# Kernel tuning notes

Measured on AMD Instinct MI355X. Metric: run time of the kernel, lower is better.

The kernel has to match this reference:

```python
import jax, jax.numpy as jnp
import numpy as np

D_IN = 2048
D_LATENT = 16384
BATCH = 4096
K = 64


def setup_inputs() -> dict:
    key = jax.random.key(0)
    k1, k2, k3 = jax.random.split(key, 3)
    s_enc = 1.0 / np.sqrt(D_IN)
    s_dec = 1.0 / np.sqrt(D_LATENT)
    return {
        "x": jax.random.normal(k1, (BATCH, D_IN), dtype=jnp.float32),
        "W_enc": jax.random.normal(k2, (D_LATENT, D_IN), dtype=jnp.float32) * s_enc,
        "b_enc": jnp.zeros((D_LATENT,), dtype=jnp.float32),
        "W_dec": jax.random.normal(k3, (D_IN, D_LATENT), dtype=jnp.float32) * s_dec,
        "b_dec": jnp.zeros((D_IN,), dtype=jnp.float32),
        "k": K,
    }


def reference(x, W_enc, b_enc, W_dec, b_dec, k):
    # encode: dense GEMM + ReLU  -> h: [B, d_latent]
    h = jax.nn.relu(jnp.einsum("bd,ld->bl", x, W_enc) + b_enc)
    # top-k masking over latent dim (dim=1)
    _, idx = jax.lax.top_k(h, k)  # idx: [B, k]
    B = h.shape[0]
    mask = jnp.zeros(h.shape, dtype=bool).at[jnp.arange(B)[:, None], idx].set(True)
    h_topk = jnp.where(mask, h, jnp.zeros((), dtype=h.dtype))
    # decode: GEMM through sparse latents
    x_hat = jnp.einsum("bl,dl->bd", h_topk, W_dec) + b_dec
    return x_hat, h, h_topk
```

## Files before the change

### kernel.cpp

```cpp
#include <hip/hip_runtime.h>
#include <cstdint>

#define DIN   2048
#define DLAT  16384
#define NB    4096
#define KSEL  64
#define MAXC  128

typedef unsigned short u16;
typedef unsigned int   u32;
typedef __attribute__((ext_vector_type(8))) short short8;
typedef __attribute__((ext_vector_type(4))) float f32x4;

#define GLOAD_LDS16(g, l)                                              \
    __builtin_amdgcn_global_load_lds(                                  \
        (const __attribute__((address_space(1))) void*)(g),            \
        (__attribute__((address_space(3))) void*)(l), 16, 0, 0)

__device__ __forceinline__ u32 f32_to_bf16(u32 u)
{
    u += 0x7FFFu + ((u >> 16) & 1u);
    return u >> 16;
}

__global__ __launch_bounds__(256)
void cvt_f32_bf16_kernel(const float* __restrict__ in, u16* __restrict__ out, int n8)
{
    const int i = blockIdx.x * 256 + threadIdx.x;
    if (i >= n8) return;
    const float4* p = reinterpret_cast<const float4*>(in) + (size_t)i * 2;
    const float4 a = p[0], b = p[1];
    const float v[8] = {a.x, a.y, a.z, a.w, b.x, b.y, b.z, b.w};
    u32 r[8];
#pragma unroll
    for (int j = 0; j < 8; ++j) r[j] = f32_to_bf16(__float_as_uint(v[j]));
    uint4 o;
    o.x = r[0] | (r[1] << 16);
    o.y = r[2] | (r[3] << 16);
    o.z = r[4] | (r[5] << 16);
    o.w = r[6] | (r[7] << 16);
    reinterpret_cast<uint4*>(out)[i] = o;
}

__global__ __launch_bounds__(512, 2)
void sae_encode_mfma512(const u16* __restrict__ XB, const u16* __restrict__ WB,
                        const float* __restrict__ benc, float* __restrict__ H)
{
    __shared__ __align__(16) u16 lds[2 * 16384];

    const int tid = threadIdx.x;
    const int wv  = tid >> 6;
    const int ln  = tid & 63;
    const int wm  = wv >> 2;
    const int wn  = wv & 3;
    const int fr  = ln & 15;
    const int fq  = ln >> 4;

    const int b   = blockIdx.x;
    const int wg  = (b & 7) * 128 + (b >> 3);
    const int m_blk = wg & 15;
    const int n_blk = wg >> 4;
    const size_t bm = (size_t)m_blk * 256;
    const size_t bn = (size_t)n_blk * 256;

    const int   srow  = tid >> 2;
    const int   sslot = (tid & 3) ^ ((tid >> 3) & 3);
    const u16* aS = XB + (bm + srow) * DIN + sslot * 8;
    const u16* bS = WB + (bn + srow) * DIN + sslot * 8;

    auto STAGE = [&](int kt, int bi) {
        const int c = kt * 32;
        GLOAD_LDS16(aS + c,                       &lds[bi * 16384 + wv * 512]);
        GLOAD_LDS16(aS + c + (size_t)128 * DIN,   &lds[bi * 16384 + 4096 + wv * 512]);
        GLOAD_LDS16(bS + c,                       &lds[bi * 16384 + 8192 + wv * 512]);
        GLOAD_LDS16(bS + c + (size_t)128 * DIN,   &lds[bi * 16384 + 12288 + wv * 512]);
    };

    f32x4 acc[8][4];
#pragma unroll
    for (int i = 0; i < 8; ++i)
#pragma unroll
        for (int j = 0; j < 4; ++j) acc[i][j] = (f32x4)0.0f;

    const int sw = (fq ^ ((fr >> 1) & 3)) * 8;

    STAGE(0, 0);
    asm volatile("s_waitcnt vmcnt(0)" ::: "memory");
    __builtin_amdgcn_s_barrier();
    asm volatile("" ::: "memory");

    for (int t = 0; t < 64; ++t) {
        const int rbase = (t & 1) * 16384;
        short8 a[8], bb[4];
#pragma unroll
        for (int mi = 0; mi < 8; ++mi)
            a[mi] = *reinterpret_cast<const short8*>(
                &lds[rbase + (wm * 128 + mi * 16 + fr) * 32 + sw]);
#pragma unroll
        for (int ni = 0; ni < 4; ++ni)
            bb[ni] = *reinterpret_cast<const short8*>(
                &lds[rbase + 8192 + (wn * 64 + ni * 16 + fr) * 32 + sw]);

        if (t < 63) STAGE(t + 1, (t + 1) & 1);

        __builtin_amdgcn_s_setprio(1);
#pragma unroll
        for (int mi = 0; mi < 8; ++mi)
#pragma unroll
            for (int ni = 0; ni < 4; ++ni)
                acc[mi][ni] = __builtin_amdgcn_mfma_f32_16x16x32_bf16(
                    a[mi], bb[ni], acc[mi][ni], 0, 0, 0);
        __builtin_amdgcn_s_setprio(0);

        asm volatile("s_waitcnt vmcnt(0)" ::: "memory");
        __builtin_amdgcn_s_barrier();
        asm volatile("" ::: "memory");
    }

#pragma unroll
    for (int ni = 0; ni < 4; ++ni) {
        const size_t col = bn + wn * 64 + ni * 16 + fr;
        const float be = benc[col];
#pragma unroll
        for (int mi = 0; mi < 8; ++mi) {
            const size_t r0 = bm + wm * 128 + mi * 16 + fq * 4;
            const f32x4 v = acc[mi][ni];
#pragma unroll
            for (int j = 0; j < 4; ++j)
                H[(r0 + j) * DLAT + col] = fmaxf(v[j] + be, 0.0f);
        }
    }
}

__global__ __launch_bounds__(256, 4)
void sae_encode_kernel(const float* __restrict__ X, const float* __restrict__ W,
                       const float* __restrict__ benc, float* __restrict__ H)
{
    __shared__ float As[32][132];
    __shared__ float Bs[32][132];

    const int tid  = threadIdx.x;
    const int bm   = blockIdx.y * 128;
    const int bn   = blockIdx.x * 128;

    const int wave = tid >> 6;
    const int lane = tid & 63;
    const int tm   = ((wave >> 1) << 3) + (lane >> 3);
    const int tn   = ((wave &  1) << 3) + (lane &  7);

    float acc[8][8];
#pragma unroll
    for (int i = 0; i < 8; ++i)
#pragma unroll
        for (int j = 0; j < 8; ++j) acc[i][j] = 0.0f;

    const int lrow = tid >> 1;
    const int lcol = (tid & 1) << 4;

    const float* xptr = X + (size_t)(bm + lrow) * DIN + lcol;
    const float* wptr = W + (size_t)(bn + lrow) * DIN + lcol;

    for (int k0 = 0; k0 < DIN; k0 += 32) {
#pragma unroll
        for (int i = 0; i < 4; ++i) {
            const float4 av = *reinterpret_cast<const float4*>(xptr + k0 + 4 * i);
            const float4 bv = *reinterpret_cast<const float4*>(wptr + k0 + 4 * i);
            const int kk = lcol + 4 * i;
            As[kk + 0][lrow] = av.x; As[kk + 1][lrow] = av.y;
            As[kk + 2][lrow] = av.z; As[kk + 3][lrow] = av.w;
            Bs[kk + 0][lrow] = bv.x; Bs[kk + 1][lrow] = bv.y;
            Bs[kk + 2][lrow] = bv.z; Bs[kk + 3][lrow] = bv.w;
        }
        __syncthreads();

#pragma unroll 8
        for (int k = 0; k < 32; ++k) {
            const float4 a0 = *reinterpret_cast<const float4*>(&As[k][tm * 8]);
            const float4 a1 = *reinterpret_cast<const float4*>(&As[k][tm * 8 + 4]);
            const float4 b0 = *reinterpret_cast<const float4*>(&Bs[k][tn * 8]);
            const float4 b1 = *reinterpret_cast<const float4*>(&Bs[k][tn * 8 + 4]);
            const float a[8] = {a0.x, a0.y, a0.z, a0.w, a1.x, a1.y, a1.z, a1.w};
            const float b[8] = {b0.x, b0.y, b0.z, b0.w, b1.x, b1.y, b1.z, b1.w};
#pragma unroll
            for (int i = 0; i < 8; ++i)
#pragma unroll
                for (int j = 0; j < 8; ++j)
                    acc[i][j] = fmaf(a[i], b[j], acc[i][j]);
        }
        __syncthreads();
    }

#pragma unroll
    for (int i = 0; i < 8; ++i) {
        float* orow = H + (size_t)(bm + tm * 8 + i) * DLAT + bn + tn * 8;
#pragma unroll
        for (int j = 0; j < 8; j += 4) {
            float4 o;
            o.x = fmaxf(acc[i][j + 0] + benc[bn + tn * 8 + j + 0], 0.0f);
            o.y = fmaxf(acc[i][j + 1] + benc[bn + tn * 8 + j + 1], 0.0f);
            o.z = fmaxf(acc[i][j + 2] + benc[bn + tn * 8 + j + 2], 0.0f);
            o.w = fmaxf(acc[i][j + 3] + benc[bn + tn * 8 + j + 3], 0.0f);
            *reinterpret_cast<float4*>(orow + j) = o;
        }
    }
}

__device__ __forceinline__ int blk_scan256(int v, volatile int* wsum,
                                           int ln, int wv, int& total)
{
#pragma unroll
    for (int off = 1; off < 64; off <<= 1) {
        const int n = __shfl_up(v, off, 64);
        if (ln >= off) v += n;
    }
    if (ln == 63) wsum[wv] = v;
    __syncthreads();
    int add = 0;
#pragma unroll
    for (int c = 0; c < 3; ++c) if (c < wv) add += wsum[c];
    total = wsum[0] + wsum[1] + wsum[2] + wsum[3];
    __syncthreads();
    return v + add;
}

template <bool WRITE_LISTS>
__global__ __launch_bounds__(256)
void sae_topk_kernel(const float* __restrict__ H, const float* __restrict__ X,
                     const float* __restrict__ Wenc, const float* __restrict__ benc,
                     float* __restrict__ Ht, int* __restrict__ sidx,
                     float* __restrict__ sval, float band)
{
    __shared__ __align__(16) float xs[DIN];
    __shared__ u32  hist[4][256];
    __shared__ int  scan_[256];
    __shared__ int  wsum[4];
    __shared__ int  sh_bin, sh_above;
    __shared__ int           cand_idx[MAXC];
    __shared__ float         cand_val[MAXC];
    __shared__ unsigned char cand_sel[MAXC];
    __shared__ float psum[32][6];

    const int tid = threadIdx.x;
    const int wv  = tid >> 6;
    const int ln  = tid & 63;
    const int row = blockIdx.x;
    const u32* __restrict__ hrow =
        reinterpret_cast<const u32*>(H) + (size_t)row * DLAT;

    {
        const float4* xp = reinterpret_cast<const float4*>(X + (size_t)row * DIN);
        reinterpret_cast<float4*>(xs)[tid * 2 + 0] = xp[tid * 2 + 0];
        reinterpret_cast<float4*>(xs)[tid * 2 + 1] = xp[tid * 2 + 1];
    }

    u32 v[64];
#pragma unroll
    for (int j = 0; j < 16; ++j) {
        const uint4 q = *reinterpret_cast<const uint4*>(hrow + j * 1024 + tid * 4);
        v[j * 4 + 0] = q.x; v[j * 4 + 1] = q.y;
        v[j * 4 + 2] = q.z; v[j * 4 + 3] = q.w;
    }

    u32 prefix = 0, msk = 0;
    int kk = KSEL;
    for (int pass = 0; pass < 4; ++pass) {
        const int shift = 24 - 8 * pass;
        hist[0][tid] = 0; hist[1][tid] = 0; hist[2][tid] = 0; hist[3][tid] = 0;
        __syncthreads();
#pragma unroll
        for (int e = 0; e < 64; ++e) {
            const u32 x = v[e];
            if (x != 0u && (x & msk) == prefix)
                atomicAdd(&hist[wv][(x >> shift) & 255u], 1u);
        }
        __syncthreads();
        int val = (int)(hist[0][255 - tid] + hist[1][255 - tid] +
                        hist[2][255 - tid] + hist[3][255 - tid]);
#pragma unroll
        for (int off = 1; off < 64; off <<= 1) {
            const int n = __shfl_up(val, off, 64);
            if (ln >= off) val += n;
        }
        if (ln == 63) wsum[wv] = val;
        __syncthreads();
        int add = 0;
#pragma unroll
        for (int c = 0; c < 3; ++c) if (c < wv) add += wsum[c];
        scan_[tid] = val + add;
        __syncthreads();
        {
            const int binh = (int)(hist[0][tid] + hist[1][tid] +
                                   hist[2][tid] + hist[3][tid]);
            const int ge = scan_[255 - tid];
            const int gt = ge - binh;
            if (gt < kk && ge >= kk) { sh_bin = tid; sh_above = gt; }
        }
        __syncthreads();
        prefix |= ((u32)sh_bin) << shift;
        msk    |= 0xFFu << shift;
        kk     -= sh_above;
        __syncthreads();
    }

    const float Tf = __uint_as_float(prefix);
    const float hi = Tf + band;
    const float lo = Tf - band;

    int c_safe = 0, c_band = 0;
#pragma unroll
    for (int e = 0; e < 64; ++e) {
        const float f = __uint_as_float(v[e]);
        c_safe += (f > hi) ? 1 : 0;
        c_band += (f >= lo && f <= hi) ? 1 : 0;
    }

    int S;
    (void)blk_scan256(c_safe, wsum, ln, wv, S);
    int totC;
    const int bincl = blk_scan256(c_band, wsum, ln, wv, totC);
    const int bexc  = bincl - c_band;
    int C = totC;
    if (C > MAXC) C = MAXC;
    int need = KSEL - S;
    if (need > C) need = C;

    {
        int bpos = bexc;
#pragma unroll
        for (int e = 0; e < 64; ++e) {
            const float f = __uint_as_float(v[e]);
            if (f >= lo && f <= hi) {
                if (bpos < MAXC)
                    cand_idx[bpos] = (e >> 2) * 1024 + tid * 4 + (e & 3);
                ++bpos;
            }
        }
    }
    __syncthreads();

    const int g = tid >> 3;
    const int p = tid & 7;
    for (int c0 = 0; c0 < C; c0 += 32) {
        const int ci = c0 + g;
        if (ci < C && p < 6) {
            const int li = cand_idx[ci];
            const float* __restrict__ wr = Wenc + (size_t)li * DIN;
            const int ks = (p < 4) ? p * 384 : 1536 + (p - 4) * 256;
            const int ke = ks + ((p < 4) ? 384 : 256);
            float s = 0.0f;
            for (int k = ks; k < ke; k += 4) {
                const float4 w4 = *reinterpret_cast<const float4*>(wr + k);
                const float4 x4 = *reinterpret_cast<const float4*>(xs + k);
                s = fmaf(x4.x, w4.x, s);
                s = fmaf(x4.y, w4.y, s);
                s = fmaf(x4.z, w4.z, s);
                s = fmaf(x4.w, w4.w, s);
            }
            psum[g][p] = s;
        }
        __syncthreads();
        if (ci < C && p == 0) {
            float total = 0.0f;
#pragma unroll
            for (int q = 0; q < 6; ++q)
                total = __fadd_rn(total, psum[g][q]);
            total = __fadd_rn(total, benc[cand_idx[ci]]);
            cand_val[ci] = fmaxf(total, 0.0f);
        }
        __syncthreads();
    }

    if (tid < C) {
        const float val = cand_val[tid];
        int r = 0;
        for (int m = 0; m < C; ++m)
            r += (cand_val[m] > val || (cand_val[m] == val && m < tid)) ? 1 : 0;
        cand_sel[tid] = (r < need) ? 1 : 0;
    }
    __syncthreads();

    unsigned long long selmask = 0ull;
#pragma unroll
    for (int e = 0; e < 64; ++e) {
        const float f = __uint_as_float(v[e]);
        bool s = (f > hi);
        if (!s && f >= lo && f <= hi) {
            const int gi = (e >> 2) * 1024 + tid * 4 + (e & 3);
            for (int m = 0; m < C; ++m)
                if (cand_idx[m] == gi) { s = (cand_sel[m] != 0); break; }
        }
        if (s) selmask |= 1ull << e;
    }
    const int csel = __popcll(selmask);

    int totSel;
    const int pincl = blk_scan256(csel, wsum, ln, wv, totSel);
    int pos = pincl - csel;

    float* orow = Ht + (size_t)row * DLAT;
#pragma unroll
    for (int j = 0; j < 16; ++j) {
        float4 o;
        o.x = ((selmask >> (j * 4 + 0)) & 1) ? __uint_as_float(v[j * 4 + 0]) : 0.0f;
        o.y = ((selmask >> (j * 4 + 1)) & 1) ? __uint_as_float(v[j * 4 + 1]) : 0.0f;
        o.z = ((selmask >> (j * 4 + 2)) & 1) ? __uint_as_float(v[j * 4 + 2]) : 0.0f;
        o.w = ((selmask >> (j * 4 + 3)) & 1) ? __uint_as_float(v[j * 4 + 3]) : 0.0f;
        *reinterpret_cast<float4*>(orow + j * 1024 + tid * 4) = o;
    }
    if (WRITE_LISTS) {
#pragma unroll
        for (int e = 0; e < 64; ++e) {
            if ((selmask >> e) & 1) {
                const int gi = (e >> 2) * 1024 + tid * 4 + (e & 3);
                sidx[(size_t)row * KSEL + pos] = gi;
                sval[(size_t)row * KSEL + pos] = __uint_as_float(v[e]);
                ++pos;
            }
        }
    }
}

__global__ __launch_bounds__(256)
void sae_transpose_cvt(const float* __restrict__ W, u16* __restrict__ WT)
{
    __shared__ float t[32][65];
    const int bx = blockIdx.x * 32;
    const int by = blockIdx.y * 64;
    const int lx = threadIdx.x;
    const int ly = threadIdx.y;

    for (int r = ly; r < 64; r += 8)
        t[lx][r] = W[(size_t)(by + r) * DLAT + bx + lx];
    __syncthreads();
    for (int c = ly; c < 32; c += 8) {
        const u32 lo = f32_to_bf16(__float_as_uint(t[c][2 * lx + 0]));
        const u32 hi = f32_to_bf16(__float_as_uint(t[c][2 * lx + 1]));
        *reinterpret_cast<u32*>(WT + (size_t)(bx + c) * DIN + by + 2 * lx) =
            lo | (hi << 16);
    }
}

__global__ __launch_bounds__(512)
void sae_decode_bf16(const u16* __restrict__ WT, const int* __restrict__ sidx,
                     const float* __restrict__ sval, const float* __restrict__ bdec,
                     float* __restrict__ xhat)
{
    __shared__ int   si[KSEL];
    __shared__ float sv[KSEL];
    const int row = blockIdx.x;
    const int tid = threadIdx.x;
    if (tid < KSEL) {
        si[tid] = sidx[(size_t)row * KSEL + tid];
        sv[tid] = sval[(size_t)row * KSEL + tid];
    }
    __syncthreads();

    const int d = tid * 4;
    float4 acc = *reinterpret_cast<const float4*>(bdec + d);
#pragma unroll 8
    for (int j = 0; j < KSEL; ++j) {
        const float f = sv[j];
        const int   l = si[j];
        const ushort4 w = *reinterpret_cast<const ushort4*>(WT + (size_t)l * DIN + d);
        acc.x = fmaf(f, __uint_as_float((u32)w.x << 16), acc.x);
        acc.y = fmaf(f, __uint_as_float((u32)w.y << 16), acc.y);
        acc.z = fmaf(f, __uint_as_float((u32)w.z << 16), acc.z);
        acc.w = fmaf(f, __uint_as_float((u32)w.w << 16), acc.w);
    }
    *reinterpret_cast<float4*>(xhat + (size_t)row * DIN + d) = acc;
}

__global__ __launch_bounds__(512)
void sae_decode_f32(const float* __restrict__ Wd, const int* __restrict__ sidx,
                    const float* __restrict__ sval, const float* __restrict__ bdec,
                    float* __restrict__ xhat)
{
    __shared__ int   si[KSEL];
    __shared__ float sv[KSEL];
    const int row = blockIdx.x;
    const int tid = threadIdx.x;
    if (tid < KSEL) {
        si[tid] = sidx[(size_t)row * KSEL + tid];
        sv[tid] = sval[(size_t)row * KSEL + tid];
    }
    __syncthreads();

    const int d = tid * 4;
    float4 acc = *reinterpret_cast<const float4*>(bdec + d);
#pragma unroll 4
    for (int j = 0; j < KSEL; ++j) {
        const float f = sv[j];
        const int   l = si[j];
        acc.x = fmaf(f, Wd[(size_t)(d + 0) * DLAT + l], acc.x);
        acc.y = fmaf(f, Wd[(size_t)(d + 1) * DLAT + l], acc.y);
        acc.z = fmaf(f, Wd[(size_t)(d + 2) * DLAT + l], acc.z);
        acc.w = fmaf(f, Wd[(size_t)(d + 3) * DLAT + l], acc.w);
    }
    *reinterpret_cast<float4*>(xhat + (size_t)row * DIN + d) = acc;
}

__global__ __launch_bounds__(512)
void sae_decode_nows_kernel(const float* __restrict__ Ht, const float* __restrict__ Wd,
                            const float* __restrict__ bdec, float* __restrict__ xhat)
{
    __shared__ int   si[KSEL];
    __shared__ float sv[KSEL];
    __shared__ unsigned cnt;
    const int row = blockIdx.x;
    const int tid = threadIdx.x;
    if (tid == 0) cnt = 0;
    __syncthreads();
    for (int i = tid; i < DLAT; i += 512) {
        const float v = Ht[(size_t)row * DLAT + i];
        if (v != 0.0f) {
            const unsigned p = atomicAdd(&cnt, 1u);
            if (p < KSEL) { si[p] = i; sv[p] = v; }
        }
    }
    __syncthreads();
    const unsigned n = cnt < (unsigned)KSEL ? cnt : (unsigned)KSEL;
    const int d = tid * 4;
    float4 acc = *reinterpret_cast<const float4*>(bdec + d);
    for (unsigned j = 0; j < n; ++j) {
        const float f = sv[j];
        const int   l = si[j];
        acc.x = fmaf(f, Wd[(size_t)(d + 0) * DLAT + l], acc.x);
        acc.y = fmaf(f, Wd[(size_t)(d + 1) * DLAT + l], acc.y);
        acc.z = fmaf(f, Wd[(size_t)(d + 2) * DLAT + l], acc.z);
        acc.w = fmaf(f, Wd[(size_t)(d + 3) * DLAT + l], acc.w);
    }
    *reinterpret_cast<float4*>(xhat + (size_t)row * DIN + d) = acc;
}

extern "C" void kernel_launch(void* const* d_in, const int* in_sizes, int n_in,
                              void* d_out, int out_size, void* d_ws, size_t ws_size,
                              hipStream_t stream)
{
    const float* x     = (const float*)d_in[0];
    const float* W_enc = (const float*)d_in[1];
    const float* b_enc = (const float*)d_in[2];
    const float* W_dec = (const float*)d_in[3];
    const float* b_dec = (const float*)d_in[4];

    float* xhat  = (float*)d_out;
    float* h     = xhat + (size_t)NB * DIN;
    float* htopk = h + (size_t)NB * DLAT;

    const size_t LIST_BYTES = 2097152ull;
    const size_t WT_BYTES   = 2ull * DLAT * DIN;
    const size_t XB_BYTES   = 2ull * NB * DIN;
    const size_t WB_BYTES   = 2ull * DLAT * DIN;
    const size_t XB_OFF     = LIST_BYTES + WT_BYTES;
    const size_t WB_OFF     = XB_OFF + XB_BYTES;

    int*   sp_idx = (int*)d_ws;
    float* sp_val = (float*)((char*)d_ws + (LIST_BYTES / 2));
    u16*   WT     = (u16*)((char*)d_ws + LIST_BYTES);
    u16*   xb     = (u16*)((char*)d_ws + XB_OFF);
    u16*   wb     = (u16*)((char*)d_ws + WB_OFF);

    const bool have_lists = ws_size >= LIST_BYTES;
    const bool have_wt    = ws_size >= LIST_BYTES + WT_BYTES;
    const bool have_mfma  = ws_size >= WB_OFF + WB_BYTES;

    const float band = have_mfma ? 0.03f : 2e-4f;

    if (have_wt) {
        sae_transpose_cvt<<<dim3(DLAT / 32, DIN / 64), dim3(32, 8), 0, stream>>>(W_dec, WT);
    }

    if (have_mfma) {
        cvt_f32_bf16_kernel<<<(NB * DIN / 8 + 255) / 256, 256, 0, stream>>>(x, xb, NB * DIN / 8);
        cvt_f32_bf16_kernel<<<(DLAT * DIN / 8 + 255) / 256, 256, 0, stream>>>(W_enc, wb, DLAT * DIN / 8);
        sae_encode_mfma512<<<(NB / 256) * (DLAT / 256), 512, 0, stream>>>(xb, wb, b_enc, h);
    } else {
        sae_encode_kernel<<<dim3(DLAT / 128, NB / 128), 256, 0, stream>>>(x, W_enc, b_enc, h);
    }

    if (have_lists) {
        sae_topk_kernel<true><<<NB, 256, 0, stream>>>(h, x, W_enc, b_enc, htopk, sp_idx, sp_val, band);
        if (have_wt) {
            sae_decode_bf16<<<NB, 512, 0, stream>>>(WT, sp_idx, sp_val, b_dec, xhat);
        } else {
            sae_decode_f32<<<NB, 512, 0, stream>>>(W_dec, sp_idx, sp_val, b_dec, xhat);
        }
    } else {
        sae_topk_kernel<false><<<NB, 256, 0, stream>>>(h, x, W_enc, b_enc, htopk, nullptr, nullptr, band);
        sae_decode_nows_kernel<<<NB, 512, 0, stream>>>(htopk, W_dec, b_dec, xhat);
    }
}
```

Baseline: 939.8 us.

## Restructure encode GEMM into multi-phase pipelined loop with deeper prefetch

The encode GEMM kernel now stages 64-wide K tiles in four 32-wide half-chunks across a 128KB double buffer. Each iteration is split into four MFMA phases, and the global-to-LDS loads for future tiles are interleaved between them under partial vmcnt waits. This replaces the single wait-all-then-barrier per K step and is meant to hide load latency behind compute. The cost is 128KB of LDS per block, which may limit occupancy to one block per CU despite launch_bounds(512,2), and the hand-counted vmcnt values are fragile.

```diff
diff --git a/kernel.cpp b/kernel.cpp
--- a/kernel.cpp
+++ b/kernel.cpp
@@ -43,10 +43,10 @@
 }
 
 __global__ __launch_bounds__(512, 2)
-void sae_encode_mfma512(const u16* __restrict__ XB, const u16* __restrict__ WB,
-                        const float* __restrict__ benc, float* __restrict__ H)
-{
-    __shared__ __align__(16) u16 lds[2 * 16384];
+void sae_encode_8ph(const u16* __restrict__ XB, const u16* __restrict__ WB,
+                    const float* __restrict__ benc, float* __restrict__ H)
+{
+    __shared__ __align__(16) u16 lds[65536];
 
     const int tid = threadIdx.x;
     const int wv  = tid >> 6;
@@ -63,17 +63,17 @@
     const size_t bm = (size_t)m_blk * 256;
     const size_t bn = (size_t)n_blk * 256;
 
-    const int   srow  = tid >> 2;
-    const int   sslot = (tid & 3) ^ ((tid >> 3) & 3);
-    const u16* aS = XB + (bm + srow) * DIN + sslot * 8;
-    const u16* bS = WB + (bn + srow) * DIN + sslot * 8;
-
-    auto STAGE = [&](int kt, int bi) {
-        const int c = kt * 32;
-        GLOAD_LDS16(aS + c,                       &lds[bi * 16384 + wv * 512]);
-        GLOAD_LDS16(aS + c + (size_t)128 * DIN,   &lds[bi * 16384 + 4096 + wv * 512]);
-        GLOAD_LDS16(bS + c,                       &lds[bi * 16384 + 8192 + wv * 512]);
-        GLOAD_LDS16(bS + c + (size_t)128 * DIN,   &lds[bi * 16384 + 12288 + wv * 512]);
+    const int sslot = (ln & 3) ^ ((ln >> 3) & 3);
+    const int srow  = wv * 16 + (ln >> 2);
+    const u16* aSrc = XB + (bm + srow) * (size_t)DIN + sslot * 8;
+    const u16* bSrc = WB + (bn + srow) * (size_t)DIN + sslot * 8;
+    const size_t rowStep = (size_t)128 * DIN;
+
+    auto STG = [&](int mat, int tile, int kkh) {
+        const u16* s0 = (mat ? bSrc : aSrc) + tile * 64 + kkh * 32;
+        const int dst = (tile & 1) * 32768 + mat * 16384 + kkh * 8192 + wv * 512;
+        GLOAD_LDS16(s0,           &lds[dst]);
+        GLOAD_LDS16(s0 + rowStep, &lds[dst + 4096]);
     };
 
     f32x4 acc[8][4];
@@ -82,39 +82,85 @@
 #pragma unroll
         for (int j = 0; j < 4; ++j) acc[i][j] = (f32x4)0.0f;
 
-    const int sw = (fq ^ ((fr >> 1) & 3)) * 8;
-
-    STAGE(0, 0);
-    asm volatile("s_waitcnt vmcnt(0)" ::: "memory");
-    __builtin_amdgcn_s_barrier();
-    asm volatile("" ::: "memory");
-
-    for (int t = 0; t < 64; ++t) {
-        const int rbase = (t & 1) * 16384;
-        short8 a[8], bb[4];
+    const int swb = (fq ^ ((fr >> 1) & 3)) * 8;
+    const int arow0 = wm * 128 + fr;
+    const int brow0 = wn * 64 + fr;
+
+    STG(0, 0, 0); STG(1, 0, 0);
+    STG(0, 0, 1); STG(1, 0, 1);
+    STG(0, 1, 0); STG(1, 1, 0);
+
+    short8 aR[8], bX[2], bY[2];
+
+    for (int g = 0; g < 32; ++g) {
+        const int buf = (g & 1) * 32768;
+
+        if (g < 31) asm volatile("s_waitcnt vmcnt(8)" ::: "memory");
+        else        asm volatile("s_waitcnt vmcnt(4)" ::: "memory");
+        __builtin_amdgcn_s_barrier();
 #pragma unroll
         for (int mi = 0; mi < 8; ++mi)
-            a[mi] = *reinterpret_cast<const short8*>(
-                &lds[rbase + (wm * 128 + mi * 16 + fr) * 32 + sw]);
-#pragma unroll
-        for (int ni = 0; ni < 4; ++ni)
-            bb[ni] = *reinterpret_cast<const short8*>(
-                &lds[rbase + 8192 + (wn * 64 + ni * 16 + fr) * 32 + sw]);
-
-        if (t < 63) STAGE(t + 1, (t + 1) & 1);
-
+            aR[mi] = *reinterpret_cast<const short8*>(
+                &lds[buf + (arow0 + mi * 16) * 32 + swb]);
+        bX[0] = *reinterpret_cast<const short8*>(&lds[buf + 16384 + (brow0 +  0) * 32 + swb]);
+        bX[1] = *reinterpret_cast<const short8*>(&lds[buf + 16384 + (brow0 + 16) * 32 + swb]);
+        if (g < 31) { STG(0, g + 1, 1); STG(1, g + 1, 1); }
+        asm volatile("s_waitcnt lgkmcnt(0)" ::: "memory");
+        __builtin_amdgcn_sched_barrier(0);
         __builtin_amdgcn_s_setprio(1);
 #pragma unroll
+        for (int mi = 0; mi < 8; ++mi) {
+            acc[mi][0] = __builtin_amdgcn_mfma_f32_16x16x32_bf16(aR[mi], bX[0], acc[mi][0], 0, 0, 0);
+            acc[mi][1] = __builtin_amdgcn_mfma_f32_16x16x32_bf16(aR[mi], bX[1], acc[mi][1], 0, 0, 0);
+        }
+        __builtin_amdgcn_s_setprio(0);
+
+        __builtin_amdgcn_s_barrier();
+        bY[0] = *reinterpret_cast<const short8*>(&lds[buf + 16384 + (brow0 + 32) * 32 + swb]);
+        bY[1] = *reinterpret_cast<const short8*>(&lds[buf + 16384 + (brow0 + 48) * 32 + swb]);
+        if (g < 30) STG(0, g + 2, 0);
+        asm volatile("s_waitcnt lgkmcnt(0)" ::: "memory");
+        __builtin_amdgcn_sched_barrier(0);
+        __builtin_amdgcn_s_setprio(1);
+#pragma unroll
+        for (int mi = 0; mi < 8; ++mi) {
+            acc[mi][2] = __builtin_amdgcn_mfma_f32_16x16x32_bf16(aR[mi], bY[0], acc[mi][2], 0, 0, 0);
+            acc[mi][3] = __builtin_amdgcn_mfma_f32_16x16x32_bf16(aR[mi], bY[1], acc[mi][3], 0, 0, 0);
+        }
+        __builtin_amdgcn_s_setprio(0);
+
+        if (g < 30)       asm volatile("s_waitcnt vmcnt(10)" ::: "memory");
+        else if (g == 30) asm volatile("s_waitcnt vmcnt(8)"  ::: "memory");
+        else              asm volatile("s_waitcnt vmcnt(0)"  ::: "memory");
+        __builtin_amdgcn_s_barrier();
+#pragma unroll
         for (int mi = 0; mi < 8; ++mi)
-#pragma unroll
-            for (int ni = 0; ni < 4; ++ni)
-                acc[mi][ni] = __builtin_amdgcn_mfma_f32_16x16x32_bf16(
-                    a[mi], bb[ni], acc[mi][ni], 0, 0, 0);
+            aR[mi] = *reinterpret_cast<const short8*>(
+                &lds[buf + 8192 + (arow0 + mi * 16) * 32 + swb]);
+        bY[0] = *reinterpret_cast<const short8*>(&lds[buf + 24576 + (brow0 + 32) * 32 + swb]);
+        bY[1] = *reinterpret_cast<const short8*>(&lds[buf + 24576 + (brow0 + 48) * 32 + swb]);
+        if (g < 30) STG(1, g + 2, 0);
+        asm volatile("s_waitcnt lgkmcnt(0)" ::: "memory");
+        __builtin_amdgcn_sched_barrier(0);
+        __builtin_amdgcn_s_setprio(1);
+#pragma unroll
+        for (int mi = 0; mi < 8; ++mi) {
+            acc[mi][2] = __builtin_amdgcn_mfma_f32_16x16x32_bf16(aR[mi], bY[0], acc[mi][2], 0, 0, 0);
+            acc[mi][3] = __builtin_amdgcn_mfma_f32_16x16x32_bf16(aR[mi], bY[1], acc[mi][3], 0, 0, 0);
+        }
         __builtin_amdgcn_s_setprio(0);
 
-        asm volatile("s_waitcnt vmcnt(0)" ::: "memory");
-        __builtin_amdgcn_s_barrier();
-        asm volatile("" ::: "memory");
+        bX[0] = *reinterpret_cast<const short8*>(&lds[buf + 24576 + (brow0 +  0) * 32 + swb]);
+        bX[1] = *reinterpret_cast<const short8*>(&lds[buf + 24576 + (brow0 + 16) * 32 + swb]);
+        asm volatile("s_waitcnt lgkmcnt(0)" ::: "memory");
+        __builtin_amdgcn_sched_barrier(0);
+        __builtin_amdgcn_s_setprio(1);
+#pragma unroll
+        for (int mi = 0; mi < 8; ++mi) {
+            acc[mi][0] = __builtin_amdgcn_mfma_f32_16x16x32_bf16(aR[mi], bX[0], acc[mi][0], 0, 0, 0);
+            acc[mi][1] = __builtin_amdgcn_mfma_f32_16x16x32_bf16(aR[mi], bX[1], acc[mi][1], 0, 0, 0);
+        }
+        __builtin_amdgcn_s_setprio(0);
     }
 
 #pragma unroll
@@ -572,7 +618,7 @@
     if (have_mfma) {
         cvt_f32_bf16_kernel<<<(NB * DIN / 8 + 255) / 256, 256, 0, stream>>>(x, xb, NB * DIN / 8);
         cvt_f32_bf16_kernel<<<(DLAT * DIN / 8 + 255) / 256, 256, 0, stream>>>(W_enc, wb, DLAT * DIN / 8);
-        sae_encode_mfma512<<<(NB / 256) * (DLAT / 256), 512, 0, stream>>>(xb, wb, b_enc, h);
+        sae_encode_8ph<<<(NB / 256) * (DLAT / 256), 512, 0, stream>>>(xb, wb, b_enc, h);
     } else {
         sae_encode_kernel<<<dim3(DLAT / 128, NB / 128), 256, 0, stream>>>(x, W_enc, b_enc, h);
     }
```

Measured after the change: 881.7 us. 1.07x faster.
